# Kernel optimization log

Measured on AMD Instinct MI355X. Metric: run time of the kernel, lower is better.

The kernel has to match this reference:

```python
import jax, jax.numpy as jnp
import numpy as np

N = 4096      # num nodes
E = 131072    # num edges
D = 128       # embed dim (in=out)
HID = 16      # kan hidden dim
G, K = 4, 3   # KAN grid_size / spline_order (GCN + FFN kans)
GA, KA = 2, 1 # attention KANLinear grid_size / spline_order
H, HD = 8, 16 # heads, head_dim

def make_grid(in_f, g, k):
    h = 2.0 / g
    pts = (np.arange(-k, g + k + 1) * h - 1.0).astype(np.float32)  # [g+2k+1]
    return jnp.asarray(np.tile(pts[None, :], (in_f, 1)))            # [in_f, g+2k+1]

GRID_D = make_grid(D, G, K)
GRID_H = make_grid(HID, G, K)
GRID_A = make_grid(D, GA, KA)

def b_splines(x, grid, k):
    # x: [n, in] -> B-spline bases [n, in, g+k] via Cox-de-Boor recursion
    x = x[:, :, None]
    g = grid[None]
    bases = ((x >= g[..., :-1]) & (x < g[..., 1:])).astype(x.dtype)
    for j in range(1, k + 1):
        bases = ((x - g[..., :-(j + 1)]) / (g[..., j:-1] - g[..., :-(j + 1)]) * bases[..., :-1]
                 + (g[..., j + 1:] - x) / (g[..., j + 1:] - g[..., 1:-j]) * bases[..., 1:])
    return bases

def kan_lin(x, bw, sw, grid, k, use_silu):
    base = jax.nn.silu(x) if use_silu else x
    return base @ bw.T + jnp.einsum('nig,oig->no', b_splines(x, grid, k), sw)

def ekan2(x, bw1, sw1, bw2, sw2):
    # eKAN with layers_hidden=[D, HID, D], SiLU base activation
    h = kan_lin(x, bw1, sw1, GRID_D, K, True)
    return kan_lin(h, bw2, sw2, GRID_H, K, True)

def layer_norm(h, s, b):
    m = jnp.mean(h, axis=-1, keepdims=True)
    v = jnp.var(h, axis=-1, keepdims=True)
    return (h - m) * jax.lax.rsqrt(v + 1e-5) * s + b

def setup_inputs() -> dict:
    key = jax.random.key(0)
    ks = jax.random.split(key, 20)
    r = lambda i, shape: jax.random.normal(ks[i], shape, jnp.float32) * 0.1
    return dict(
        x=jax.random.normal(ks[0], (N, D), jnp.float32),
        edge_index=jax.random.randint(ks[1], (2, E), 0, N),
        gcn_bw1=r(2, (HID, D)), gcn_sw1=r(3, (HID, D, G + K)),
        gcn_bw2=r(4, (D, HID)), gcn_sw2=r(5, (D, HID, G + K)),
        q_bw=r(6, (D, D)), q_sw=r(7, (D, D, GA + KA)),
        k_bw=r(8, (D, D)), k_sw=r(9, (D, D, GA + KA)),
        v_bw=r(10, (D, D)), v_sw=r(11, (D, D, GA + KA)),
        ffn_bw1=r(12, (HID, D)), ffn_sw1=r(13, (HID, D, G + K)),
        ffn_bw2=r(14, (D, HID)), ffn_sw2=r(15, (D, HID, G + K)),
        ln1_s=jnp.ones(D), ln1_b=jnp.zeros(D),
        ln2_s=jnp.ones(D), ln2_b=jnp.zeros(D),
        ln3_s=jnp.ones(D), ln3_b=jnp.zeros(D),
    )

def reference(x, edge_index, gcn_bw1, gcn_sw1, gcn_bw2, gcn_sw2,
              q_bw, q_sw, k_bw, k_sw, v_bw, v_sw,
              ffn_bw1, ffn_sw1, ffn_bw2, ffn_sw2,
              ln1_s, ln1_b, ln2_s, ln2_b, ln3_s, ln3_b):
    n = x.shape[0]
    # ---- local GCN-KAN branch: KAN(A_hat x) ----
    loops = jnp.arange(n)
    row = jnp.concatenate([edge_index[0], loops])  # sources (+ self-loops)
    col = jnp.concatenate([edge_index[1], loops])  # targets
    w = jnp.ones(row.shape[0], x.dtype)
    deg = jax.ops.segment_sum(w, row, num_segments=n)
    dis = jnp.where(deg > 0, deg ** -0.5, 0.0)
    norm = dis[row] * w * dis[col]
    agg = jax.ops.segment_sum(norm[:, None] * x[row], col, num_segments=n)  # [n, D]
    h_local = ekan2(agg, gcn_bw1, gcn_sw1, gcn_bw2, gcn_sw2)
    h_local = layer_norm(x + h_local, ln1_s, ln1_b)
    # ---- global KAN multi-head attention branch ----
    Q = kan_lin(x, q_bw, q_sw, GRID_A, KA, False).reshape(n, H, HD)
    Kv = kan_lin(x, k_bw, k_sw, GRID_A, KA, False).reshape(n, H, HD)
    V = kan_lin(x, v_bw, v_sw, GRID_A, KA, False).reshape(n, H, HD)
    scores = jnp.einsum('nhd,mhd->hnm', Q, Kv) / np.sqrt(HD)  # [H, n, n]
    attn = jax.nn.softmax(scores, axis=-1)
    h_attn = jnp.einsum('hnm,mhd->nhd', attn, V).reshape(n, D)
    h_attn = layer_norm(x + h_attn, ln2_s, ln2_b)
    # ---- combine + KAN feed-forward ----
    h = h_local + h_attn
    out = layer_norm(h + ekan2(h, ffn_bw1, ffn_sw1, ffn_bw2, ffn_sw2), ln3_s, ln3_b)
    return out
```

## Files before the change

### kernel.cpp

```cpp
#include <hip/hip_runtime.h>

typedef unsigned short u16;
typedef unsigned int u32;

#define D_ 128
#define HID_ 16
#define NH_ 8
#define HD_ 16
#define PSTRIDE 17

#define WE_W1G 0
#define WE_W2G 16384
#define WE_W1F 32768
#define WE_W2F 49152
#define WE_TOTAL 65536

#define KROW 24
#define VROW 136
#define PROW 40

typedef __attribute__((ext_vector_type(8))) short bfrag;
typedef __attribute__((ext_vector_type(4))) float ffrag;


__device__ __forceinline__ float bf2f(u16 u) {
    union { u32 i; float f; } v; v.i = ((u32)u) << 16; return v.f;
}
__device__ __forceinline__ u16 f2bf(float f) {
    u32 x = __float_as_uint(f);
    u32 r = (x + 0x7fffu + ((x >> 16) & 1u)) >> 16;
    return (u16)r;
}
__device__ __forceinline__ float rdf(const void* p, int i, bool bf) {
    return bf ? bf2f(((const u16*)p)[i]) : ((const float*)p)[i];
}

__device__ __forceinline__ u32 probe_stat(const u16* p) {
    for (int i = 0; i < 128; i++) {
        u16 u = p[i];
        int e = (u >> 7) & 0xFF;
        int m = u & 0x7F;
        bool zero = (e == 0) && (m == 0);
        bool sane = zero || (e >= 97 && e <= 147);
        if (!sane) return 0u;
    }
    return 1u;
}

__global__ void k_detect(const void* x,
                         const void* gbw1, const void* gsw1, const void* gbw2, const void* gsw2,
                         const void* qbw, const void* qsw, const void* kbw, const void* ksw,
                         const void* vbw, const void* vsw,
                         const void* fbw1, const void* fsw1, const void* fbw2, const void* fsw2,
                         const void* l1s, const void* l1b, const void* l2s, const void* l2b,
                         const void* l3s, const void* l3b,
                         u32* flags) {
    int t = threadIdx.x;
    const void* ptrs[21] = {x, gbw1, gsw1, gbw2, gsw2, qbw, qsw, kbw, ksw, vbw, vsw,
                            fbw1, fsw1, fbw2, fsw2, l1s, l1b, l2s, l2b, l3s, l3b};
    if (t < 21) {
        u32 f = 0;
        if (t == 15 || t == 17 || t == 19) {
            f = (((const u32*)ptrs[t])[0] != 0x3F800000u) ? 1u : 0u;
        } else if (t == 16 || t == 18 || t == 20) {
            f = 0;
        } else {
            f = probe_stat((const u16*)ptrs[t]);
        }
        flags[t] = f;
    }
    __syncthreads();
    if (t == 16 || t == 18 || t == 20) flags[t] = flags[t - 1];
}

__device__ __forceinline__ float cub_seg(float s) {
    if (s < 0.0f || s >= 4.0f) return 0.0f;
    if (s < 1.0f) return s * s * s * (1.0f / 6.0f);
    if (s < 2.0f) { float r = s - 1.0f; return (1.0f + 3.0f * r + 3.0f * r * r - 3.0f * r * r * r) * (1.0f / 6.0f); }
    if (s < 3.0f) { float r = s - 2.0f; return (4.0f - 6.0f * r * r + 3.0f * r * r * r) * (1.0f / 6.0f); }
    float q = 4.0f - s; return q * q * q * (1.0f / 6.0f);
}
__device__ __forceinline__ float lin_seg(float s) {
    if (s < 0.0f || s >= 2.0f) return 0.0f;
    return (s < 1.0f) ? s : (2.0f - s);
}

__device__ __forceinline__ float bsum(float v, float* tmp) {
#pragma unroll
    for (int off = 1; off < 64; off <<= 1) v += __shfl_xor(v, off, 64);
    __syncthreads();
    if ((threadIdx.x & 63) == 0) tmp[threadIdx.x >> 6] = v;
    __syncthreads();
    return tmp[0] + tmp[1];
}

__device__ __forceinline__ uint4 feat8(float a) {
    float si = a / (1.0f + __expf(-a));
    float u = (a + 2.5f) * 2.0f;
    float b0 = cub_seg(u), b1 = cub_seg(u - 1.0f), b2 = cub_seg(u - 2.0f), b3 = cub_seg(u - 3.0f);
    float b4 = cub_seg(u - 4.0f), b5 = cub_seg(u - 5.0f), b6 = cub_seg(u - 6.0f);
    uint4 r;
    r.x = (u32)f2bf(si) | ((u32)f2bf(b0) << 16);
    r.y = (u32)f2bf(b1) | ((u32)f2bf(b2) << 16);
    r.z = (u32)f2bf(b3) | ((u32)f2bf(b4) << 16);
    r.w = (u32)f2bf(b5) | ((u32)f2bf(b6) << 16);
    return r;
}

__global__ void k_conv3(const void* __restrict__ x,
                        const void* l1s, const void* l1b, const void* l2s,
                        const void* l2b, const void* l3s, const void* l3b,
                        const u32* __restrict__ flags,
                        float* __restrict__ xin, float* __restrict__ lnp,
                        u16* __restrict__ F, int N) {
    int total = N * D_ + 768;
    bool bfx = flags[0] != 0;
    for (int i = blockIdx.x * 256 + threadIdx.x; i < total; i += gridDim.x * 256) {
        if (i < N * D_) {
            float xv = rdf(x, i, bfx);
            xin[i] = xv;
            float u = xv + 2.0f;
            u32 lo = (u32)f2bf(xv) | ((u32)f2bf(lin_seg(u)) << 16);
            u32 hi = (u32)f2bf(lin_seg(u - 1.0f)) | ((u32)f2bf(lin_seg(u - 2.0f)) << 16);
            ((uint2*)F)[i] = make_uint2(lo, hi);
        } else {
            int j = i - N * D_;
            int sel = j >> 7, k = j & 127;
            const void* p = sel == 0 ? l1s : sel == 1 ? l1b : sel == 2 ? l2s
                         : sel == 3 ? l2b : sel == 4 ? l3s : l3b;
            lnp[j] = rdf(p, k, flags[15 + sel] != 0);
        }
    }
}

__global__ void k_pack(const void* gbw1, const void* gsw1, const void* gbw2, const void* gsw2,
                       const void* fbw1, const void* fsw1, const void* fbw2, const void* fsw2,
                       const void* qbw, const void* qsw, const void* kbw, const void* ksw,
                       const void* vbw, const void* vsw,
                       const u32* __restrict__ flags,
                       u16* __restrict__ Web, u16* __restrict__ Wb) {
    int t = blockIdx.x * 256 + threadIdx.x;
    if (t < 8192) {
        int seg = t >> 11, i = t & 2047;
        const void* bw = seg == 0 ? gbw1 : seg == 1 ? gbw2 : seg == 2 ? fbw1 : fbw2;
        const void* sw = seg == 0 ? gsw1 : seg == 1 ? gsw2 : seg == 2 ? fsw1 : fsw2;
        int fb = seg == 0 ? 1 : seg == 1 ? 3 : seg == 2 ? 11 : 13;
        bool bwbf = flags[fb] != 0, swbf = flags[fb + 1] != 0;
        u16* dst = Web + (size_t)seg * 16384 + (size_t)i * 8;
        dst[0] = f2bf(rdf(bw, i, bwbf));
#pragma unroll
        for (int g = 0; g < 7; g++) dst[1 + g] = f2bf(rdf(sw, i * 7 + g, swbf));
    } else if (t < 8192 + 49152) {
        int uu = t - 8192;
        int seg = uu >> 14, i = uu & 16383;
        const void* bw = seg == 0 ? qbw : seg == 1 ? kbw : vbw;
        const void* sw = seg == 0 ? qsw : seg == 1 ? ksw : vsw;
        int fb = 5 + seg * 2;
        bool bwbf = flags[fb] != 0, swbf = flags[fb + 1] != 0;
        float sc = (seg == 0) ? 0.25f : 1.0f;
        u16* dst = Wb + (size_t)seg * 65536 + (size_t)i * 4;
        dst[0] = f2bf(rdf(bw, i, bwbf) * sc);
#pragma unroll
        for (int g = 0; g < 3; g++) dst[1 + g] = f2bf(rdf(sw, i * 3 + g, swbf) * sc);
    }
}

__global__ void k_zero(int* __restrict__ cnt, int* __restrict__ fill,
                       int* __restrict__ degi, int N) {
    int i = blockIdx.x * 256 + threadIdx.x;
    if (i < N) { cnt[i] = 0; fill[i] = 0; degi[i] = 0; }
}
__global__ void k_count(const int* __restrict__ ei, int* __restrict__ cnt,
                        int* __restrict__ degi, int E) {
    int e = blockIdx.x * 256 + threadIdx.x;
    if (e < E) {
        atomicAdd(&degi[ei[e]], 1);
        atomicAdd(&cnt[ei[E + e]], 1);
    }
}
__global__ __launch_bounds__(1024) void k_scan(const int* __restrict__ cnt,
                                               const int* __restrict__ degi,
                                               int* __restrict__ rowptr,
                                               float* __restrict__ dis, int N) {
    __shared__ int s[1024];
    int t = threadIdx.x;
    int base = t * 4;
    int a[4];
#pragma unroll
    for (int k = 0; k < 4; k++) a[k] = (base + k < N) ? cnt[base + k] : 0;
    int loc = a[0] + a[1] + a[2] + a[3];
    s[t] = loc;
    __syncthreads();
    for (int off = 1; off < 1024; off <<= 1) {
        int v = (t >= off) ? s[t - off] : 0;
        __syncthreads();
        s[t] += v;
        __syncthreads();
    }
    int ex = s[t] - loc;
    int run = ex;
#pragma unroll
    for (int k = 0; k < 4; k++) {
        if (base + k < N) rowptr[base + k] = run;
        run += a[k];
    }
    if (t == 1023) rowptr[N] = s[1023];
#pragma unroll
    for (int k = 0; k < 4; k++)
        if (base + k < N) dis[base + k] = rsqrtf((float)degi[base + k] + 1.0f);
}
__global__ void k_fill(const int* __restrict__ ei, const int* __restrict__ rowptr,
                       int* __restrict__ fill, int* __restrict__ elist, int E) {
    int e = blockIdx.x * 256 + threadIdx.x;
    if (e < E) {
        int r = ei[e], c = ei[E + e];
        int pos = rowptr[c] + atomicAdd(&fill[c], 1);
        elist[pos] = r;
    }
}

__global__ __launch_bounds__(128) void k_gcn(const int* __restrict__ rowptr,
        const int* __restrict__ elist, const float* __restrict__ dis,
        const float* __restrict__ xin, u16* __restrict__ Afeat) {
    int c = blockIdx.x, t = threadIdx.x;
    __shared__ int ids[128];
    __shared__ float wsh[128];
    int beg = rowptr[c], end = rowptr[c + 1];
    float acc = 0.0f;
    for (int j0 = beg; j0 < end; j0 += 128) {
        int cc = min(128, end - j0);
        __syncthreads();
        if (t < cc) {
            int rr = elist[j0 + t];
            ids[t] = rr;
            wsh[t] = dis[rr];
        }
        __syncthreads();
        for (int j = 0; j < cc; j++)
            acc += wsh[j] * xin[(size_t)ids[j] * D_ + t];
    }
    float dc = dis[c];
    float a = dc * (acc + dc * xin[(size_t)c * D_ + t]);
    ((uint4*)Afeat)[(size_t)c * D_ + t] = feat8(a);
}

__global__ __launch_bounds__(64) void k_gemm1(const u16* __restrict__ A,
        const u16* __restrict__ W1b, u16* __restrict__ hf, int N) {
    int mt = blockIdx.x;
    int lane = threadIdx.x, quad = lane >> 4, l15 = lane & 15;
    const u16* ar = A + (size_t)(mt * 16 + l15) * 1024 + quad * 8;
    const u16* br = W1b + (size_t)l15 * 1024 + quad * 8;
    ffrag acc = {0, 0, 0, 0};
#pragma unroll
    for (int ks = 0; ks < 1024; ks += 32) {
        bfrag af = *(const bfrag*)(ar + ks);
        bfrag bf = *(const bfrag*)(br + ks);
        acc = __builtin_amdgcn_mfma_f32_16x16x32_bf16(af, bf, acc, 0, 0, 0);
    }
    int nb = mt * 16 + quad * 4;
#define G1EPI(RR, COMP) { \
    uint4 fv = feat8(acc.COMP); \
    ((uint4*)hf)[((size_t)(nb + RR) * 128 + l15 * 8) >> 3] = fv; }
    G1EPI(0, x) G1EPI(1, y) G1EPI(2, z) G1EPI(3, w)
#undef G1EPI
}

__global__ __launch_bounds__(64) void k_gemm2(const u16* __restrict__ hf,
        const u16* __restrict__ W2b, const float* __restrict__ resid,
        const float* __restrict__ lns, const float* __restrict__ lnb,
        void* __restrict__ outp, const u32* __restrict__ flags, int fin, int N) {
    int mt = blockIdx.x;
    int lane = threadIdx.x, quad = lane >> 4, l15 = lane & 15;
    const u16* ar = hf + (size_t)(mt * 16 + l15) * 128 + quad * 8;
    const u16* b0 = W2b + (size_t)(0 * 16 + l15) * 128 + quad * 8;
    const u16* b1 = b0 + 16 * 128;
    const u16* b2 = b0 + 32 * 128;
    const u16* b3 = b0 + 48 * 128;
    const u16* b4 = b0 + 64 * 128;
    const u16* b5 = b0 + 80 * 128;
    const u16* b6 = b0 + 96 * 128;
    const u16* b7 = b0 + 112 * 128;
    ffrag a0 = {0,0,0,0}, a1 = {0,0,0,0}, a2 = {0,0,0,0}, a3 = {0,0,0,0};
    ffrag a4 = {0,0,0,0}, a5 = {0,0,0,0}, a6 = {0,0,0,0}, a7 = {0,0,0,0};
#pragma unroll
    for (int ks = 0; ks < 128; ks += 32) {
        bfrag af = *(const bfrag*)(ar + ks);
        a0 = __builtin_amdgcn_mfma_f32_16x16x32_bf16(af, *(const bfrag*)(b0 + ks), a0, 0, 0, 0);
        a1 = __builtin_amdgcn_mfma_f32_16x16x32_bf16(af, *(const bfrag*)(b1 + ks), a1, 0, 0, 0);
        a2 = __builtin_amdgcn_mfma_f32_16x16x32_bf16(af, *(const bfrag*)(b2 + ks), a2, 0, 0, 0);
        a3 = __builtin_amdgcn_mfma_f32_16x16x32_bf16(af, *(const bfrag*)(b3 + ks), a3, 0, 0, 0);
        a4 = __builtin_amdgcn_mfma_f32_16x16x32_bf16(af, *(const bfrag*)(b4 + ks), a4, 0, 0, 0);
        a5 = __builtin_amdgcn_mfma_f32_16x16x32_bf16(af, *(const bfrag*)(b5 + ks), a5, 0, 0, 0);
        a6 = __builtin_amdgcn_mfma_f32_16x16x32_bf16(af, *(const bfrag*)(b6 + ks), a6, 0, 0, 0);
        a7 = __builtin_amdgcn_mfma_f32_16x16x32_bf16(af, *(const bfrag*)(b7 + ks), a7, 0, 0, 0);
    }
    float ls0 = lns[l15],       lb0 = lnb[l15];
    float ls1 = lns[16 + l15],  lb1 = lnb[16 + l15];
    float ls2 = lns[32 + l15],  lb2 = lnb[32 + l15];
    float ls3 = lns[48 + l15],  lb3 = lnb[48 + l15];
    float ls4 = lns[64 + l15],  lb4 = lnb[64 + l15];
    float ls5 = lns[80 + l15],  lb5 = lnb[80 + l15];
    float ls6 = lns[96 + l15],  lb6 = lnb[96 + l15];
    float ls7 = lns[112 + l15], lb7 = lnb[112 + l15];
    bool bfo = (fin != 0) && (flags[0] != 0);
#define G2EPI(RR, COMP) { \
    int node = mt * 16 + quad * 4 + RR; \
    const float* rr_ = resid + (size_t)node * 128 + l15; \
    float v0 = a0.COMP + rr_[0];   float v1 = a1.COMP + rr_[16]; \
    float v2 = a2.COMP + rr_[32];  float v3 = a3.COMP + rr_[48]; \
    float v4 = a4.COMP + rr_[64];  float v5 = a5.COMP + rr_[80]; \
    float v6 = a6.COMP + rr_[96];  float v7 = a7.COMP + rr_[112]; \
    float s1 = ((v0 + v1) + (v2 + v3)) + ((v4 + v5) + (v6 + v7)); \
    float s2 = ((v0*v0 + v1*v1) + (v2*v2 + v3*v3)) + ((v4*v4 + v5*v5) + (v6*v6 + v7*v7)); \
    s1 += __shfl_xor(s1, 1, 64); s2 += __shfl_xor(s2, 1, 64); \
    s1 += __shfl_xor(s1, 2, 64); s2 += __shfl_xor(s2, 2, 64); \
    s1 += __shfl_xor(s1, 4, 64); s2 += __shfl_xor(s2, 4, 64); \
    s1 += __shfl_xor(s1, 8, 64); s2 += __shfl_xor(s2, 8, 64); \
    float mean = s1 * 0.0078125f; \
    float var = s2 * 0.0078125f - mean * mean; \
    float rs = rsqrtf(var + 1e-5f); \
    float y0 = (v0 - mean) * rs * ls0 + lb0; float y1 = (v1 - mean) * rs * ls1 + lb1; \
    float y2 = (v2 - mean) * rs * ls2 + lb2; float y3 = (v3 - mean) * rs * ls3 + lb3; \
    float y4 = (v4 - mean) * rs * ls4 + lb4; float y5 = (v5 - mean) * rs * ls5 + lb5; \
    float y6 = (v6 - mean) * rs * ls6 + lb6; float y7 = (v7 - mean) * rs * ls7 + lb7; \
    if (bfo) { \
        u16* ob = (u16*)outp + (size_t)node * 128 + l15; \
        ob[0] = f2bf(y0); ob[16] = f2bf(y1); ob[32] = f2bf(y2); ob[48] = f2bf(y3); \
        ob[64] = f2bf(y4); ob[80] = f2bf(y5); ob[96] = f2bf(y6); ob[112] = f2bf(y7); \
    } else { \
        float* ob = (float*)outp + (size_t)node * 128 + l15; \
        ob[0] = y0; ob[16] = y1; ob[32] = y2; ob[48] = y3; \
        ob[64] = y4; ob[80] = y5; ob[96] = y6; ob[112] = y7; \
    } }
    G2EPI(0, x) G2EPI(1, y) G2EPI(2, z) G2EPI(3, w)
#undef G2EPI
}

#define QKV_STORE(ACC, TL) { \
    int col = cg * 48 + (TL) * 16 + l15; \
    int mat = col >> 7, idx = col & 127; \
    u16* dstb = (mat == 0) ? Qb : (mat == 1) ? Kb : Vb; \
    size_t base = (size_t)(idx >> 4) * N * HD_ + (size_t)(idx & 15); \
    dstb[base + (size_t)(rowb + 0) * HD_] = f2bf(ACC.x); \
    dstb[base + (size_t)(rowb + 1) * HD_] = f2bf(ACC.y); \
    dstb[base + (size_t)(rowb + 2) * HD_] = f2bf(ACC.z); \
    dstb[base + (size_t)(rowb + 3) * HD_] = f2bf(ACC.w); \
}

__global__ __launch_bounds__(64) void k_qkv5(const u16* __restrict__ F,
        const u16* __restrict__ Wb,
        u16* __restrict__ Qb, u16* __restrict__ Kb, u16* __restrict__ Vb, int N) {
    int mt = blockIdx.x, cg = blockIdx.y;
    int lane = threadIdx.x, quad = lane >> 4, l15 = lane & 15;
    const u16* arow = F + (size_t)(mt * 16 + l15) * 512 + quad * 8;
    const u16* b0r = Wb + (size_t)(cg * 48 + l15) * 512 + quad * 8;
    const u16* b1r = b0r + 16 * 512;
    const u16* b2r = b0r + 32 * 512;
    ffrag a0 = {0, 0, 0, 0}, a1 = {0, 0, 0, 0}, a2 = {0, 0, 0, 0};
#pragma unroll
    for (int ks = 0; ks < 512; ks += 32) {
        bfrag af = *(const bfrag*)(arow + ks);
        bfrag bf0 = *(const bfrag*)(b0r + ks);
        bfrag bf1 = *(const bfrag*)(b1r + ks);
        bfrag bf2 = *(const bfrag*)(b2r + ks);
        a0 = __builtin_amdgcn_mfma_f32_16x16x32_bf16(af, bf0, a0, 0, 0, 0);
        a1 = __builtin_amdgcn_mfma_f32_16x16x32_bf16(af, bf1, a1, 0, 0, 0);
        a2 = __builtin_amdgcn_mfma_f32_16x16x32_bf16(af, bf2, a2, 0, 0, 0);
    }
    int rowb = mt * 16 + quad * 4;
    QKV_STORE(a0, 0)
    QKV_STORE(a1, 1)
    QKV_STORE(a2, 2)
}

#define ATTN_SCORE(QF, LACC, PBT) { \
    ffrag zz = {0.0f, 0.0f, 0.0f, 0.0f}; \
    ffrag s0 = __builtin_amdgcn_mfma_f32_16x16x32_bf16(QF, kf0, zz, 0, 0, 0); \
    ffrag s1 = __builtin_amdgcn_mfma_f32_16x16x32_bf16(QF, kf1, zz, 0, 0, 0); \
    float a0 = __expf(s0.x), a1 = __expf(s0.y), a2 = __expf(s0.z), a3 = __expf(s0.w); \
    float b0 = __expf(s1.x), b1 = __expf(s1.y), b2 = __expf(s1.z), b3 = __expf(s1.w); \
    LACC.x += a0 + b0; LACC.y += a1 + b1; LACC.z += a2 + b2; LACC.w += a3 + b3; \
    PBT[(quad * 4 + 0) * PROW + l15] = (u16)(__float_as_uint(a0) >> 16); \
    PBT[(quad * 4 + 1) * PROW + l15] = (u16)(__float_as_uint(a1) >> 16); \
    PBT[(quad * 4 + 2) * PROW + l15] = (u16)(__float_as_uint(a2) >> 16); \
    PBT[(quad * 4 + 3) * PROW + l15] = (u16)(__float_as_uint(a3) >> 16); \
    PBT[(quad * 4 + 0) * PROW + l15 + 16] = (u16)(__float_as_uint(b0) >> 16); \
    PBT[(quad * 4 + 1) * PROW + l15 + 16] = (u16)(__float_as_uint(b1) >> 16); \
    PBT[(quad * 4 + 2) * PROW + l15 + 16] = (u16)(__float_as_uint(b2) >> 16); \
    PBT[(quad * 4 + 3) * PROW + l15 + 16] = (u16)(__float_as_uint(b3) >> 16); \
}

#define ATTN_PV(OACC, PBT) { \
    bfrag pf = *(const bfrag*)(&PBT[l15 * PROW + quad * 8]); \
    OACC = __builtin_amdgcn_mfma_f32_16x16x32_bf16(pf, vf, OACC, 0, 0, 0); \
}

#define STORE_TILE(OACC, LACC, TL) { \
    int q0 = qtb + (TL) * 16 + quad * 4; \
    float* pp; \
    pp = part + ((size_t)(h * N + q0 + 0) * SPLIT + s) * PSTRIDE; \
    pp[1 + l15] = OACC.x; if (l15 == 0) pp[0] = LACC.x; \
    pp = part + ((size_t)(h * N + q0 + 1) * SPLIT + s) * PSTRIDE; \
    pp[1 + l15] = OACC.y; if (l15 == 0) pp[0] = LACC.y; \
    pp = part + ((size_t)(h * N + q0 + 2) * SPLIT + s) * PSTRIDE; \
    pp[1 + l15] = OACC.z; if (l15 == 0) pp[0] = LACC.z; \
    pp = part + ((size_t)(h * N + q0 + 3) * SPLIT + s) * PSTRIDE; \
    pp[1 + l15] = OACC.w; if (l15 == 0) pp[0] = LACC.w; \
}

__global__ __launch_bounds__(256) void k_attn8(const u16* __restrict__ Qb,
        const u16* __restrict__ Kb, const u16* __restrict__ Vb,
        float* __restrict__ part, int N, int SPLIT) {
    int s = blockIdx.x, qb = blockIdx.y, h = blockIdx.z;
    int t = threadIdx.x;
    int w = t >> 6, lane = t & 63, quad = lane >> 4, l15 = lane & 15;
    __shared__ u16 ldsK[128 * KROW + 16];
    __shared__ u16 ldsVt[16 * VROW];
    __shared__ u16 ldsP[4][4][16 * PROW];

    const u16* qrow = Qb + (size_t)h * N * HD_;
    const u16* krow = Kb + (size_t)h * N * HD_;
    const u16* vrow = Vb + (size_t)h * N * HD_;

    for (int i = t; i < (128 * KROW + 16) / 2; i += 256) ((u32*)ldsK)[i] = 0;

    int qtb = qb * 256 + w * 64;
    bfrag qz = {0, 0, 0, 0, 0, 0, 0, 0};
    bfrag qf0 = qz, qf1 = qz, qf2 = qz, qf3 = qz;
    if (quad < 2) {
        qf0 = *(const bfrag*)(qrow + (size_t)(qtb + 0 * 16 + l15) * HD_ + quad * 8);
        qf1 = *(const bfrag*)(qrow + (size_t)(qtb + 1 * 16 + l15) * HD_ + quad * 8);
        qf2 = *(const bfrag*)(qrow + (size_t)(qtb + 2 * 16 + l15) * HD_ + quad * 8);
        qf3 = *(const bfrag*)(qrow + (size_t)(qtb + 3 * 16 + l15) * HD_ + quad * 8);
    }

    ffrag o0 = {0, 0, 0, 0}, o1 = {0, 0, 0, 0}, o2 = {0, 0, 0, 0}, o3 = {0, 0, 0, 0};
    ffrag L0 = {0, 0, 0, 0}, L1 = {0, 0, 0, 0}, L2 = {0, 0, 0, 0}, L3 = {0, 0, 0, 0};
    u16* pb0 = &ldsP[w][0][0];
    u16* pb1 = &ldsP[w][1][0];
    u16* pb2 = &ldsP[w][2][0];
    u16* pb3 = &ldsP[w][3][0];

    int keys = N / SPLIT;
    int kstart0 = s * keys;
    for (int kst = 0; kst < keys; kst += 128) {
        int kg = kstart0 + kst;
        __syncthreads();
        if (t < 128) {
            const uint4* src = (const uint4*)(krow + (size_t)(kg + t) * HD_);
            uint4 a = src[0], b = src[1];
            *(uint4*)(&ldsK[t * KROW]) = a;
            *(uint4*)(&ldsK[t * KROW + 8]) = b;
        } else {
            int key = t - 128;
            const uint4* src = (const uint4*)(vrow + (size_t)(kg + key) * HD_);
            uint4 a = src[0], b = src[1];
            ldsVt[0 * VROW + key] = (u16)(a.x);  ldsVt[1 * VROW + key] = (u16)(a.x >> 16);
            ldsVt[2 * VROW + key] = (u16)(a.y);  ldsVt[3 * VROW + key] = (u16)(a.y >> 16);
            ldsVt[4 * VROW + key] = (u16)(a.z);  ldsVt[5 * VROW + key] = (u16)(a.z >> 16);
            ldsVt[6 * VROW + key] = (u16)(a.w);  ldsVt[7 * VROW + key] = (u16)(a.w >> 16);
            ldsVt[8 * VROW + key] = (u16)(b.x);  ldsVt[9 * VROW + key] = (u16)(b.x >> 16);
            ldsVt[10 * VROW + key] = (u16)(b.y); ldsVt[11 * VROW + key] = (u16)(b.y >> 16);
            ldsVt[12 * VROW + key] = (u16)(b.z); ldsVt[13 * VROW + key] = (u16)(b.z >> 16);
            ldsVt[14 * VROW + key] = (u16)(b.w); ldsVt[15 * VROW + key] = (u16)(b.w >> 16);
        }
        __syncthreads();
#pragma unroll
        for (int koff = 0; koff < 128; koff += 32) {
            bfrag kf0 = *(const bfrag*)(&ldsK[(koff + l15) * KROW + quad * 8]);
            bfrag kf1 = *(const bfrag*)(&ldsK[(koff + 16 + l15) * KROW + quad * 8]);
            bfrag vf = *(const bfrag*)(&ldsVt[l15 * VROW + koff + quad * 8]);
            ATTN_SCORE(qf0, L0, pb0)
            ATTN_SCORE(qf1, L1, pb1)
            ATTN_SCORE(qf2, L2, pb2)
            ATTN_SCORE(qf3, L3, pb3)
            __asm__ volatile("s_waitcnt lgkmcnt(0)" ::: "memory");
            ATTN_PV(o0, pb0)
            ATTN_PV(o1, pb1)
            ATTN_PV(o2, pb2)
            ATTN_PV(o3, pb3)
        }
    }

#pragma unroll
    for (int off = 1; off < 16; off <<= 1) {
        L0.x += __shfl_xor(L0.x, off, 64); L0.y += __shfl_xor(L0.y, off, 64);
        L0.z += __shfl_xor(L0.z, off, 64); L0.w += __shfl_xor(L0.w, off, 64);
        L1.x += __shfl_xor(L1.x, off, 64); L1.y += __shfl_xor(L1.y, off, 64);
        L1.z += __shfl_xor(L1.z, off, 64); L1.w += __shfl_xor(L1.w, off, 64);
        L2.x += __shfl_xor(L2.x, off, 64); L2.y += __shfl_xor(L2.y, off, 64);
        L2.z += __shfl_xor(L2.z, off, 64); L2.w += __shfl_xor(L2.w, off, 64);
        L3.x += __shfl_xor(L3.x, off, 64); L3.y += __shfl_xor(L3.y, off, 64);
        L3.z += __shfl_xor(L3.z, off, 64); L3.w += __shfl_xor(L3.w, off, 64);
    }
    STORE_TILE(o0, L0, 0)
    STORE_TILE(o1, L1, 1)
    STORE_TILE(o2, L2, 2)
    STORE_TILE(o3, L3, 3)
}

__global__ __launch_bounds__(128) void k_comb(const float* __restrict__ part,
        const float* __restrict__ xin, const float* __restrict__ hl,
        const float* __restrict__ lnp, float* __restrict__ hv,
        u16* __restrict__ Afeat, int N, int SPLIT) {
    int n = blockIdx.x, t = threadIdx.x;
    __shared__ float red[128];
    int h = t >> 4, d = t & 15;
    float L = 0.0f, O = 0.0f;
    for (int ss = 0; ss < SPLIT; ss++) {
        const float* ps = part + ((size_t)(h * N + n) * SPLIT + ss) * PSTRIDE;
        L += ps[0];
        O += ps[1 + d];
    }
    float ha = O / L;
    float r = xin[(size_t)n * D_ + t] + ha;
    float mean = bsum(r, red) * (1.0f / 128.0f);
    float c = r - mean;
    float var = bsum(c * c, red) * (1.0f / 128.0f);
    float y2 = c * rsqrtf(var + 1e-5f) * lnp[256 + t] + lnp[384 + t];
    float hvv = hl[(size_t)n * D_ + t] + y2;
    hv[(size_t)n * D_ + t] = hvv;
    ((uint4*)Afeat)[(size_t)n * D_ + t] = feat8(hvv);
}

extern "C" void kernel_launch(void* const* d_in, const int* in_sizes, int n_in,
                              void* d_out, int out_size, void* d_ws, size_t ws_size,
                              hipStream_t stream) {
    const void* x = d_in[0];
    const int* ei = (const int*)d_in[1];
    const void* gbw1 = d_in[2];
    const void* gsw1 = d_in[3];
    const void* gbw2 = d_in[4];
    const void* gsw2 = d_in[5];
    const void* qbw = d_in[6];
    const void* qsw = d_in[7];
    const void* kbw = d_in[8];
    const void* ksw = d_in[9];
    const void* vbw = d_in[10];
    const void* vsw = d_in[11];
    const void* fbw1 = d_in[12];
    const void* fsw1 = d_in[13];
    const void* fbw2 = d_in[14];
    const void* fsw2 = d_in[15];
    const void* ln1s = d_in[16];
    const void* ln1b = d_in[17];
    const void* ln2s = d_in[18];
    const void* ln2b = d_in[19];
    const void* ln3s = d_in[20];
    const void* ln3b = d_in[21];

    const int N = in_sizes[0] / D_;
    const int E = in_sizes[1] / 2;
    const size_t ND = (size_t)N * D_;

    float* wf = (float*)d_ws;
    u32* flags = (u32*)wf;
    float* lnp = wf + 32;
    float* dis = wf + 800;
    float* xin = dis + N;
    float* hl  = xin + ND;
    float* hv  = hl + ND;
    u16* Web = (u16*)(hv + ND);
    u16* Wb  = Web + WE_TOTAL;
    u16* F   = Wb + 196608;
    u16* Qb  = F + (size_t)N * 512;
    u16* Kb  = Qb + ND;
    u16* Vb  = Kb + ND;
    u16* Afeat = Vb + ND;
    u16* hf  = Afeat + (size_t)N * 1024;
    int* cnt    = (int*)(hf + ND);
    int* fill   = cnt + N;
    int* degi   = fill + N;
    int* rowptr = degi + N;
    int* elist  = rowptr + N + 1;
    float* part = (float*)(elist + E);

    size_t baseBytes = (size_t)((char*)part - (char*)d_ws);
    int SPLIT = 8;
    if (baseBytes + (size_t)NH_ * N * 8 * PSTRIDE * 4 > ws_size) SPLIT = 4;

    k_detect<<<1, 64, 0, stream>>>(x, gbw1, gsw1, gbw2, gsw2, qbw, qsw, kbw, ksw,
                                   vbw, vsw, fbw1, fsw1, fbw2, fsw2,
                                   ln1s, ln1b, ln2s, ln2b, ln3s, ln3b, flags);
    k_conv3<<<1024, 256, 0, stream>>>(x, ln1s, ln1b, ln2s, ln2b, ln3s, ln3b,
                                      flags, xin, lnp, F, N);
    k_pack<<<224, 256, 0, stream>>>(gbw1, gsw1, gbw2, gsw2, fbw1, fsw1, fbw2, fsw2,
                                    qbw, qsw, kbw, ksw, vbw, vsw, flags, Web, Wb);
    k_zero<<<(N + 255) / 256, 256, 0, stream>>>(cnt, fill, degi, N);
    k_count<<<(E + 255) / 256, 256, 0, stream>>>(ei, cnt, degi, E);
    k_scan<<<1, 1024, 0, stream>>>(cnt, degi, rowptr, dis, N);
    k_fill<<<(E + 255) / 256, 256, 0, stream>>>(ei, rowptr, fill, elist, E);
    k_gcn<<<N, 128, 0, stream>>>(rowptr, elist, dis, xin, Afeat);
    k_gemm1<<<N / 16, 64, 0, stream>>>(Afeat, Web + WE_W1G, hf, N);
    k_gemm2<<<N / 16, 64, 0, stream>>>(hf, Web + WE_W2G, xin, lnp + 0, lnp + 128,
                                       hl, flags, 0, N);
    k_qkv5<<<dim3(N / 16, 8), 64, 0, stream>>>(F, Wb, Qb, Kb, Vb, N);
    k_attn8<<<dim3(SPLIT, N / 256, NH_), 256, 0, stream>>>(Qb, Kb, Vb, part, N, SPLIT);
    k_comb<<<N, 128, 0, stream>>>(part, xin, hl, lnp, hv, Afeat, N, SPLIT);
    k_gemm1<<<N / 16, 64, 0, stream>>>(Afeat, Web + WE_W1F, hf, N);
    k_gemm2<<<N / 16, 64, 0, stream>>>(hf, Web + WE_W2F, hv, lnp + 512, lnp + 640,
                                       d_out, flags, 1, N);
}
```

Measured before the change: 249.3 us.

## Fuse eKAN GEMMs via LDS, merge zeroing into conversion, widen attention split

Merges the two eKAN GEMM kernels into one, passing the hidden B-spline features through LDS instead of a global buffer. Folds the counter-zeroing kernel into the input conversion kernel to save launches. Also packs the probability stores in the attention score step into 32-bit words and interleaves the K row mapping to match. Raises the attention key split from 8 to 16 when workspace allows, adding more partial results for the combine step to reduce.

```diff
diff --git a/kernel.cpp b/kernel.cpp
--- a/kernel.cpp
+++ b/kernel.cpp
@@ -18,6 +18,7 @@
 #define KROW 24
 #define VROW 136
 #define PROW 40
+#define HROW 136
 
 typedef __attribute__((ext_vector_type(8))) short bfrag;
 typedef __attribute__((ext_vector_type(4))) float ffrag;
@@ -107,13 +108,15 @@
     return r;
 }
 
-__global__ void k_conv3(const void* __restrict__ x,
+__global__ void k_conv4(const void* __restrict__ x,
                         const void* l1s, const void* l1b, const void* l2s,
                         const void* l2b, const void* l3s, const void* l3b,
                         const u32* __restrict__ flags,
                         float* __restrict__ xin, float* __restrict__ lnp,
-                        u16* __restrict__ F, int N) {
-    int total = N * D_ + 768;
+                        u16* __restrict__ F,
+                        int* __restrict__ cnt, int* __restrict__ fill,
+                        int* __restrict__ degi, int N) {
+    int total = N * D_ + 768 + 3 * N;
     bool bfx = flags[0] != 0;
     for (int i = blockIdx.x * 256 + threadIdx.x; i < total; i += gridDim.x * 256) {
         if (i < N * D_) {
@@ -125,10 +128,17 @@
             ((uint2*)F)[i] = make_uint2(lo, hi);
         } else {
             int j = i - N * D_;
-            int sel = j >> 7, k = j & 127;
-            const void* p = sel == 0 ? l1s : sel == 1 ? l1b : sel == 2 ? l2s
-                         : sel == 3 ? l2b : sel == 4 ? l3s : l3b;
-            lnp[j] = rdf(p, k, flags[15 + sel] != 0);
+            if (j < 768) {
+                int sel = j >> 7, k = j & 127;
+                const void* p = sel == 0 ? l1s : sel == 1 ? l1b : sel == 2 ? l2s
+                             : sel == 3 ? l2b : sel == 4 ? l3s : l3b;
+                lnp[j] = rdf(p, k, flags[15 + sel] != 0);
+            } else {
+                int j2 = j - 768;
+                if (j2 < N) cnt[j2] = 0;
+                else if (j2 < 2 * N) fill[j2 - N] = 0;
+                else degi[j2 - 2 * N] = 0;
+            }
         }
     }
 }
@@ -165,11 +175,6 @@
     }
 }
 
-__global__ void k_zero(int* __restrict__ cnt, int* __restrict__ fill,
-                       int* __restrict__ degi, int N) {
-    int i = blockIdx.x * 256 + threadIdx.x;
-    if (i < N) { cnt[i] = 0; fill[i] = 0; degi[i] = 0; }
-}
 __global__ void k_count(const int* __restrict__ ei, int* __restrict__ cnt,
                         int* __restrict__ degi, int E) {
     int e = blockIdx.x * 256 + threadIdx.x;
@@ -244,8 +249,12 @@
     ((uint4*)Afeat)[(size_t)c * D_ + t] = feat8(a);
 }
 
-__global__ __launch_bounds__(64) void k_gemm1(const u16* __restrict__ A,
-        const u16* __restrict__ W1b, u16* __restrict__ hf, int N) {
+__global__ __launch_bounds__(64) void k_ekan_mm(const u16* __restrict__ A,
+        const u16* __restrict__ W1b, const u16* __restrict__ W2b,
+        const float* __restrict__ resid,
+        const float* __restrict__ lns, const float* __restrict__ lnb,
+        void* __restrict__ outp, const u32* __restrict__ flags, int fin, int N) {
+    __shared__ u16 hfL[16 * HROW];
     int mt = blockIdx.x;
     int lane = threadIdx.x, quad = lane >> 4, l15 = lane & 15;
     const u16* ar = A + (size_t)(mt * 16 + l15) * 1024 + quad * 8;
@@ -257,42 +266,27 @@
         bfrag bf = *(const bfrag*)(br + ks);
         acc = __builtin_amdgcn_mfma_f32_16x16x32_bf16(af, bf, acc, 0, 0, 0);
     }
-    int nb = mt * 16 + quad * 4;
 #define G1EPI(RR, COMP) { \
     uint4 fv = feat8(acc.COMP); \
-    ((uint4*)hf)[((size_t)(nb + RR) * 128 + l15 * 8) >> 3] = fv; }
+    *(uint4*)(&hfL[(quad * 4 + RR) * HROW + l15 * 8]) = fv; }
     G1EPI(0, x) G1EPI(1, y) G1EPI(2, z) G1EPI(3, w)
 #undef G1EPI
-}
-
-__global__ __launch_bounds__(64) void k_gemm2(const u16* __restrict__ hf,
-        const u16* __restrict__ W2b, const float* __restrict__ resid,
-        const float* __restrict__ lns, const float* __restrict__ lnb,
-        void* __restrict__ outp, const u32* __restrict__ flags, int fin, int N) {
-    int mt = blockIdx.x;
-    int lane = threadIdx.x, quad = lane >> 4, l15 = lane & 15;
-    const u16* ar = hf + (size_t)(mt * 16 + l15) * 128 + quad * 8;
-    const u16* b0 = W2b + (size_t)(0 * 16 + l15) * 128 + quad * 8;
-    const u16* b1 = b0 + 16 * 128;
-    const u16* b2 = b0 + 32 * 128;
-    const u16* b3 = b0 + 48 * 128;
-    const u16* b4 = b0 + 64 * 128;
-    const u16* b5 = b0 + 80 * 128;
-    const u16* b6 = b0 + 96 * 128;
-    const u16* b7 = b0 + 112 * 128;
+    __asm__ volatile("s_waitcnt lgkmcnt(0)" ::: "memory");
+    __builtin_amdgcn_wave_barrier();
+    const u16* b0 = W2b + (size_t)l15 * 128 + quad * 8;
     ffrag a0 = {0,0,0,0}, a1 = {0,0,0,0}, a2 = {0,0,0,0}, a3 = {0,0,0,0};
     ffrag a4 = {0,0,0,0}, a5 = {0,0,0,0}, a6 = {0,0,0,0}, a7 = {0,0,0,0};
 #pragma unroll
     for (int ks = 0; ks < 128; ks += 32) {
-        bfrag af = *(const bfrag*)(ar + ks);
-        a0 = __builtin_amdgcn_mfma_f32_16x16x32_bf16(af, *(const bfrag*)(b0 + ks), a0, 0, 0, 0);
-        a1 = __builtin_amdgcn_mfma_f32_16x16x32_bf16(af, *(const bfrag*)(b1 + ks), a1, 0, 0, 0);
-        a2 = __builtin_amdgcn_mfma_f32_16x16x32_bf16(af, *(const bfrag*)(b2 + ks), a2, 0, 0, 0);
-        a3 = __builtin_amdgcn_mfma_f32_16x16x32_bf16(af, *(const bfrag*)(b3 + ks), a3, 0, 0, 0);
-        a4 = __builtin_amdgcn_mfma_f32_16x16x32_bf16(af, *(const bfrag*)(b4 + ks), a4, 0, 0, 0);
-        a5 = __builtin_amdgcn_mfma_f32_16x16x32_bf16(af, *(const bfrag*)(b5 + ks), a5, 0, 0, 0);
-        a6 = __builtin_amdgcn_mfma_f32_16x16x32_bf16(af, *(const bfrag*)(b6 + ks), a6, 0, 0, 0);
-        a7 = __builtin_amdgcn_mfma_f32_16x16x32_bf16(af, *(const bfrag*)(b7 + ks), a7, 0, 0, 0);
+        bfrag af = *(const bfrag*)(&hfL[l15 * HROW + quad * 8 + ks]);
+        a0 = __builtin_amdgcn_mfma_f32_16x16x32_bf16(af, *(const bfrag*)(b0 + 0 * 2048 + ks), a0, 0, 0, 0);
+        a1 = __builtin_amdgcn_mfma_f32_16x16x32_bf16(af, *(const bfrag*)(b0 + 1 * 2048 + ks), a1, 0, 0, 0);
+        a2 = __builtin_amdgcn_mfma_f32_16x16x32_bf16(af, *(const bfrag*)(b0 + 2 * 2048 + ks), a2, 0, 0, 0);
+        a3 = __builtin_amdgcn_mfma_f32_16x16x32_bf16(af, *(const bfrag*)(b0 + 3 * 2048 + ks), a3, 0, 0, 0);
+        a4 = __builtin_amdgcn_mfma_f32_16x16x32_bf16(af, *(const bfrag*)(b0 + 4 * 2048 + ks), a4, 0, 0, 0);
+        a5 = __builtin_amdgcn_mfma_f32_16x16x32_bf16(af, *(const bfrag*)(b0 + 5 * 2048 + ks), a5, 0, 0, 0);
+        a6 = __builtin_amdgcn_mfma_f32_16x16x32_bf16(af, *(const bfrag*)(b0 + 6 * 2048 + ks), a6, 0, 0, 0);
+        a7 = __builtin_amdgcn_mfma_f32_16x16x32_bf16(af, *(const bfrag*)(b0 + 7 * 2048 + ks), a7, 0, 0, 0);
     }
     float ls0 = lns[l15],       lb0 = lnb[l15];
     float ls1 = lns[16 + l15],  lb1 = lnb[16 + l15];
@@ -380,14 +374,11 @@
     float a0 = __expf(s0.x), a1 = __expf(s0.y), a2 = __expf(s0.z), a3 = __expf(s0.w); \
     float b0 = __expf(s1.x), b1 = __expf(s1.y), b2 = __expf(s1.z), b3 = __expf(s1.w); \
     LACC.x += a0 + b0; LACC.y += a1 + b1; LACC.z += a2 + b2; LACC.w += a3 + b3; \
-    PBT[(quad * 4 + 0) * PROW + l15] = (u16)(__float_as_uint(a0) >> 16); \
-    PBT[(quad * 4 + 1) * PROW + l15] = (u16)(__float_as_uint(a1) >> 16); \
-    PBT[(quad * 4 + 2) * PROW + l15] = (u16)(__float_as_uint(a2) >> 16); \
-    PBT[(quad * 4 + 3) * PROW + l15] = (u16)(__float_as_uint(a3) >> 16); \
-    PBT[(quad * 4 + 0) * PROW + l15 + 16] = (u16)(__float_as_uint(b0) >> 16); \
-    PBT[(quad * 4 + 1) * PROW + l15 + 16] = (u16)(__float_as_uint(b1) >> 16); \
-    PBT[(quad * 4 + 2) * PROW + l15 + 16] = (u16)(__float_as_uint(b2) >> 16); \
-    PBT[(quad * 4 + 3) * PROW + l15 + 16] = (u16)(__float_as_uint(b3) >> 16); \
+    u32* pw = (u32*)PBT; \
+    pw[(quad * 4 + 0) * (PROW / 2) + l15] = (__float_as_uint(a0) >> 16) | (__float_as_uint(b0) & 0xFFFF0000u); \
+    pw[(quad * 4 + 1) * (PROW / 2) + l15] = (__float_as_uint(a1) >> 16) | (__float_as_uint(b1) & 0xFFFF0000u); \
+    pw[(quad * 4 + 2) * (PROW / 2) + l15] = (__float_as_uint(a2) >> 16) | (__float_as_uint(b2) & 0xFFFF0000u); \
+    pw[(quad * 4 + 3) * (PROW / 2) + l15] = (__float_as_uint(a3) >> 16) | (__float_as_uint(b3) & 0xFFFF0000u); \
 }
 
 #define ATTN_PV(OACC, PBT) { \
@@ -408,7 +399,7 @@
     pp[1 + l15] = OACC.w; if (l15 == 0) pp[0] = LACC.w; \
 }
 
-__global__ __launch_bounds__(256) void k_attn8(const u16* __restrict__ Qb,
+__global__ __launch_bounds__(256) void k_attn9(const u16* __restrict__ Qb,
         const u16* __restrict__ Kb, const u16* __restrict__ Vb,
         float* __restrict__ part, int N, int SPLIT) {
     int s = blockIdx.x, qb = blockIdx.y, h = blockIdx.z;
@@ -467,8 +458,8 @@
         __syncthreads();
 #pragma unroll
         for (int koff = 0; koff < 128; koff += 32) {
-            bfrag kf0 = *(const bfrag*)(&ldsK[(koff + l15) * KROW + quad * 8]);
-            bfrag kf1 = *(const bfrag*)(&ldsK[(koff + 16 + l15) * KROW + quad * 8]);
+            bfrag kf0 = *(const bfrag*)(&ldsK[(koff + 2 * l15) * KROW + quad * 8]);
+            bfrag kf1 = *(const bfrag*)(&ldsK[(koff + 2 * l15 + 1) * KROW + quad * 8]);
             bfrag vf = *(const bfrag*)(&ldsVt[l15 * VROW + koff + quad * 8]);
             ATTN_SCORE(qf0, L0, pb0)
             ATTN_SCORE(qf1, L1, pb1)
@@ -567,8 +558,7 @@
     u16* Kb  = Qb + ND;
     u16* Vb  = Kb + ND;
     u16* Afeat = Vb + ND;
-    u16* hf  = Afeat + (size_t)N * 1024;
-    int* cnt    = (int*)(hf + ND);
+    int* cnt    = (int*)(Afeat + (size_t)N * 1024);
     int* fill   = cnt + N;
     int* degi   = fill + N;
     int* rowptr = degi + N;
@@ -576,28 +566,26 @@
     float* part = (float*)(elist + E);
 
     size_t baseBytes = (size_t)((char*)part - (char*)d_ws);
-    int SPLIT = 8;
+    int SPLIT = 16;
+    if (baseBytes + (size_t)NH_ * N * 16 * PSTRIDE * 4 > ws_size) SPLIT = 8;
     if (baseBytes + (size_t)NH_ * N * 8 * PSTRIDE * 4 > ws_size) SPLIT = 4;
 
     k_detect<<<1, 64, 0, stream>>>(x, gbw1, gsw1, gbw2, gsw2, qbw, qsw, kbw, ksw,
                                    vbw, vsw, fbw1, fsw1, fbw2, fsw2,
                                    ln1s, ln1b, ln2s, ln2b, ln3s, ln3b, flags);
-    k_conv3<<<1024, 256, 0, stream>>>(x, ln1s, ln1b, ln2s, ln2b, ln3s, ln3b,
-                                      flags, xin, lnp, F, N);
+    k_conv4<<<1024, 256, 0, stream>>>(x, ln1s, ln1b, ln2s, ln2b, ln3s, ln3b,
+                                      flags, xin, lnp, F, cnt, fill, degi, N);
     k_pack<<<224, 256, 0, stream>>>(gbw1, gsw1, gbw2, gsw2, fbw1, fsw1, fbw2, fsw2,
                                     qbw, qsw, kbw, ksw, vbw, vsw, flags, Web, Wb);
-    k_zero<<<(N + 255) / 256, 256, 0, stream>>>(cnt, fill, degi, N);
     k_count<<<(E + 255) / 256, 256, 0, stream>>>(ei, cnt, degi, E);
     k_scan<<<1, 1024, 0, stream>>>(cnt, degi, rowptr, dis, N);
     k_fill<<<(E + 255) / 256, 256, 0, stream>>>(ei, rowptr, fill, elist, E);
     k_gcn<<<N, 128, 0, stream>>>(rowptr, elist, dis, xin, Afeat);
-    k_gemm1<<<N / 16, 64, 0, stream>>>(Afeat, Web + WE_W1G, hf, N);
-    k_gemm2<<<N / 16, 64, 0, stream>>>(hf, Web + WE_W2G, xin, lnp + 0, lnp + 128,
-                                       hl, flags, 0, N);
+    k_ekan_mm<<<N / 16, 64, 0, stream>>>(Afeat, Web + WE_W1G, Web + WE_W2G, xin,
+                                         lnp + 0, lnp + 128, hl, flags, 0, N);
     k_qkv5<<<dim3(N / 16, 8), 64, 0, stream>>>(F, Wb, Qb, Kb, Vb, N);
-    k_attn8<<<dim3(SPLIT, N / 256, NH_), 256, 0, stream>>>(Qb, Kb, Vb, part, N, SPLIT);
+    k_attn9<<<dim3(SPLIT, N / 256, NH_), 256, 0, stream>>>(Qb, Kb, Vb, part, N, SPLIT);
     k_comb<<<N, 128, 0, stream>>>(part, xin, hl, lnp, hv, Afeat, N, SPLIT);
-    k_gemm1<<<N / 16, 64, 0, stream>>>(Afeat, Web + WE_W1F, hf, N);
-    k_gemm2<<<N / 16, 64, 0, stream>>>(hf, Web + WE_W2F, hv, lnp + 512, lnp + 640,
-                                       d_out, flags, 1, N);
-}
+    k_ekan_mm<<<N / 16, 64, 0, stream>>>(Afeat, Web + WE_W1F, Web + WE_W2F, hv,
+                                         lnp + 512, lnp + 640, d_out, flags, 1, N);
+}
```

Measured after the change: 247.5 us. About the same (-0.7%).
